# Kernel tuning notes

Hardware: AMD Instinct MI355X
Metric: run time of the kernel (lower is better)

## Reference

```python
import jax, jax.numpy as jnp
import numpy as np

B, L, D = 4, 512, 128

def setup_inputs() -> dict:
    key = jax.random.key(0)
    k1, k2, k3, k4 = jax.random.split(key, 4)
    s = 1.0 / np.sqrt(D)
    return {
        "inp": jax.random.normal(k1, (B, L, D), dtype=jnp.float32),
        "Wu": jax.random.normal(k2, (D, D), dtype=jnp.float32) * s,
        "Ww": jax.random.normal(k3, (D, D), dtype=jnp.float32) * s,
        "Wv": jax.random.normal(k4, (1, D), dtype=jnp.float32) * s,
    }

def reference(inp, Wu, Ww, Wv):
    # inp: (B,L,D); torch Linear weights are (out,in), so y = x @ W.T
    qu = inp @ Wu.T                      # (B,L,D), u(inp)
    kw = inp @ Ww.T                      # (B,L,D), w(inp)
    # qu.unsqueeze(1) -> broadcast over i; kw.unsqueeze(2) -> broadcast over j
    # h[b,i,j,:] = tanh(u(inp)[b,j] + w(inp)[b,i])   (dropout = identity in eval)
    h = jnp.tanh(qu[:, None, :, :] + kw[:, :, None, :])   # (B,L,L,D)
    score = jnp.einsum('bijd,d->bij', h, Wv[0])           # (B,L,L)
    attn = jax.nn.softmax(score, axis=2)                  # softmax over keys j
    out = jnp.einsum('bij,bjd->bid', attn, inp)           # bmm(attn, inp)
    return out, attn
```

## Files before the change

### kernel.cpp

```cpp
#include <hip/hip_runtime.h>

#define BD 128
#define SL 512
#define NB 4

__device__ __forceinline__ float rcp_fast(float x) { return __builtin_amdgcn_rcpf(x); }

__global__ __launch_bounds__(256) void k_tr(const float* __restrict__ Wu,
                                            const float* __restrict__ Ww,
                                            float* __restrict__ WuT,
                                            float* __restrict__ WwT) {
    int idx = blockIdx.x * 256 + threadIdx.x;
    int k = idx >> 7, o = idx & 127;
    WuT[idx] = Wu[o * BD + k];
    WwT[idx] = Ww[o * BD + k];
}

__global__ __launch_bounds__(256) void k_qk(const float* __restrict__ inp,
                                            const float* __restrict__ WuT,
                                            const float* __restrict__ WwT,
                                            float* __restrict__ Equ,
                                            float* __restrict__ Ekw) {
    __shared__ float sx[4][BD];
    const int t = threadIdx.x, m = t >> 7, o = t & 127;
    const int r0 = blockIdx.x * 4;
    const int b  = r0 >> 9;
    const int l0 = r0 & (SL - 1);

    #pragma unroll
    for (int h = 0; h < 2; ++h) {
        int id = h * 256 + t;
        sx[id >> 7][id & 127] = inp[(size_t)r0 * BD + id];
    }
    __syncthreads();

    const float* WT = m ? WwT : WuT;
    float acc[4] = {0.f, 0.f, 0.f, 0.f};
    #pragma unroll 8
    for (int k = 0; k < BD; ++k) {
        float w = WT[k * BD + o];
        #pragma unroll
        for (int rr = 0; rr < 4; ++rr)
            acc[rr] = fmaf(sx[rr][k], w, acc[rr]);
    }

    if (m == 0) {
        #pragma unroll
        for (int rr = 0; rr < 4; ++rr)
            Equ[(((size_t)b * 32 + (o >> 2)) * SL + (l0 + rr)) * 4 + (o & 3)] =
                __expf(2.f * acc[rr]);
    } else {
        #pragma unroll
        for (int rr = 0; rr < 4; ++rr)
            Ekw[(size_t)(r0 + rr) * BD + o] = __expf(2.f * acc[rr]);
    }
}

__global__ __launch_bounds__(1024, 4) void k_attn(const float* __restrict__ inp,
                                                  const float* __restrict__ Wv,
                                                  const float* __restrict__ Equ,
                                                  const float* __restrict__ Ekw,
                                                  float* __restrict__ out,
                                                  float* __restrict__ attn) {
    __shared__ float4 smem4[(SL * 8 + 15 * 8 * BD) / 4];
    float* smem  = (float*)smem4;
    float* s_pT  = smem;
    float* ovl   = smem + SL * 8;
    float4* s_e0 = (float4*)ovl;
    float4* s_e1 = ((float4*)ovl) + BD;
    float* s_wv  = ovl + 1024;
    float* s_ap  = ovl + 1152;
    float* s_red = ovl + 5248;
    float* s_fin = ovl;

    const int t  = threadIdx.x;
    const int b  = blockIdx.x >> 6;
    const int i0 = (blockIdx.x & 63) * 8;

    if (t < BD) {
        const float* ek = Ekw + ((size_t)b * SL + i0) * BD + t;
        s_e0[t] = make_float4(ek[0], ek[BD], ek[2 * BD], ek[3 * BD]);
        s_e1[t] = make_float4(ek[4 * BD], ek[5 * BD], ek[6 * BD], ek[7 * BD]);
        s_wv[t] = Wv[t];
    }
    __syncthreads();

    const int j = t & 511, dh = t >> 9;
    const float4* equ4 = (const float4*)(Equ + (size_t)b * BD * SL);
    float a[8] = {0.f, 0.f, 0.f, 0.f, 0.f, 0.f, 0.f, 0.f};
    #pragma unroll 4
    for (int cc = 0; cc < 16; ++cc) {
        int c = dh * 16 + cc;
        float4 q = equ4[c * SL + j];
        float qs[4] = {q.x, q.y, q.z, q.w};
        #pragma unroll
        for (int dd = 0; dd < 4; ++dd) {
            int d = c * 4 + dd;
            float4 e0 = s_e0[d];
            float4 e1 = s_e1[d];
            float  w  = s_wv[d];
            float  qd = qs[dd];
            a[0] = fmaf(w, rcp_fast(fmaf(qd, e0.x, 1.f)), a[0]);
            a[1] = fmaf(w, rcp_fast(fmaf(qd, e0.y, 1.f)), a[1]);
            a[2] = fmaf(w, rcp_fast(fmaf(qd, e0.z, 1.f)), a[2]);
            a[3] = fmaf(w, rcp_fast(fmaf(qd, e0.w, 1.f)), a[3]);
            a[4] = fmaf(w, rcp_fast(fmaf(qd, e1.x, 1.f)), a[4]);
            a[5] = fmaf(w, rcp_fast(fmaf(qd, e1.y, 1.f)), a[5]);
            a[6] = fmaf(w, rcp_fast(fmaf(qd, e1.z, 1.f)), a[6]);
            a[7] = fmaf(w, rcp_fast(fmaf(qd, e1.w, 1.f)), a[7]);
        }
    }

    const int ro = dh * 4;
    const int wo = 4 - ro;
    #pragma unroll
    for (int ii = 0; ii < 4; ++ii) s_ap[(wo + ii) * SL + j] = a[wo + ii];
    __syncthreads();
    float af[4];
    #pragma unroll
    for (int ii = 0; ii < 4; ++ii) af[ii] = a[ro + ii] + s_ap[(ro + ii) * SL + j];

    const int w8 = j >> 6;
    float mn[4];
    #pragma unroll
    for (int ii = 0; ii < 4; ++ii) mn[ii] = af[ii];
    #pragma unroll
    for (int off = 32; off > 0; off >>= 1) {
        #pragma unroll
        for (int ii = 0; ii < 4; ++ii) mn[ii] = fminf(mn[ii], __shfl_xor(mn[ii], off, 64));
    }
    if ((j & 63) == 0) {
        #pragma unroll
        for (int ii = 0; ii < 4; ++ii) s_red[(dh * 4 + ii) * 8 + w8] = mn[ii];
    }
    __syncthreads();
    #pragma unroll
    for (int ii = 0; ii < 4; ++ii) {
        float4 r0 = *(const float4*)&s_red[(dh * 4 + ii) * 8];
        float4 r1 = *(const float4*)&s_red[(dh * 4 + ii) * 8 + 4];
        mn[ii] = fminf(fminf(fminf(r0.x, r0.y), fminf(r0.z, r0.w)),
                       fminf(fminf(r1.x, r1.y), fminf(r1.z, r1.w)));
    }

    float p[4], sm[4];
    #pragma unroll
    for (int ii = 0; ii < 4; ++ii) { p[ii] = __expf(-2.f * (af[ii] - mn[ii])); sm[ii] = p[ii]; }
    #pragma unroll
    for (int off = 32; off > 0; off >>= 1) {
        #pragma unroll
        for (int ii = 0; ii < 4; ++ii) sm[ii] += __shfl_xor(sm[ii], off, 64);
    }
    __syncthreads();
    if ((j & 63) == 0) {
        #pragma unroll
        for (int ii = 0; ii < 4; ++ii) s_red[(dh * 4 + ii) * 8 + w8] = sm[ii];
    }
    __syncthreads();
    float n[4];
    #pragma unroll
    for (int ii = 0; ii < 4; ++ii) {
        float4 r0 = *(const float4*)&s_red[(dh * 4 + ii) * 8];
        float4 r1 = *(const float4*)&s_red[(dh * 4 + ii) * 8 + 4];
        float rs = rcp_fast((r0.x + r0.y) + (r0.z + r0.w) + (r1.x + r1.y) + (r1.z + r1.w));
        n[ii] = p[ii] * rs;
        attn[((size_t)b * SL + i0 + ro + ii) * SL + j] = n[ii];
    }
    ((float4*)s_pT)[j * 2 + dh] = make_float4(n[0], n[1], n[2], n[3]);
    __syncthreads();

    const int g   = t >> 6;
    const int ln  = t & 63;
    const int dq  = ln & 31;
    const int ig4 = ln >> 5;
    const float4* inp4 = (const float4*)(inp + (size_t)b * SL * BD);
    float4 acc[4];
    #pragma unroll
    for (int ii = 0; ii < 4; ++ii) acc[ii] = make_float4(0.f, 0.f, 0.f, 0.f);
    #pragma unroll 4
    for (int jj = 0; jj < 32; ++jj) {
        int jr = g * 32 + jj;
        float4 x  = inp4[jr * 32 + dq];
        float4 pp = *(const float4*)&s_pT[jr * 8 + ig4 * 4];
        acc[0].x = fmaf(pp.x, x.x, acc[0].x); acc[0].y = fmaf(pp.x, x.y, acc[0].y);
        acc[0].z = fmaf(pp.x, x.z, acc[0].z); acc[0].w = fmaf(pp.x, x.w, acc[0].w);
        acc[1].x = fmaf(pp.y, x.x, acc[1].x); acc[1].y = fmaf(pp.y, x.y, acc[1].y);
        acc[1].z = fmaf(pp.y, x.z, acc[1].z); acc[1].w = fmaf(pp.y, x.w, acc[1].w);
        acc[2].x = fmaf(pp.z, x.x, acc[2].x); acc[2].y = fmaf(pp.z, x.y, acc[2].y);
        acc[2].z = fmaf(pp.z, x.z, acc[2].z); acc[2].w = fmaf(pp.z, x.w, acc[2].w);
        acc[3].x = fmaf(pp.w, x.x, acc[3].x); acc[3].y = fmaf(pp.w, x.y, acc[3].y);
        acc[3].z = fmaf(pp.w, x.z, acc[3].z); acc[3].w = fmaf(pp.w, x.w, acc[3].w);
    }
    __syncthreads();
    if (g) {
        #pragma unroll
        for (int ii = 0; ii < 4; ++ii)
            *(float4*)&s_fin[((g - 1) * 8 + ig4 * 4 + ii) * BD + dq * 4] = acc[ii];
    }
    __syncthreads();
    if (g == 0) {
        #pragma unroll
        for (int r = 0; r < 15; ++r) {
            #pragma unroll
            for (int ii = 0; ii < 4; ++ii) {
                float4 v = *(const float4*)&s_fin[(r * 8 + ig4 * 4 + ii) * BD + dq * 4];
                acc[ii].x += v.x; acc[ii].y += v.y; acc[ii].z += v.z; acc[ii].w += v.w;
            }
        }
        #pragma unroll
        for (int ii = 0; ii < 4; ++ii)
            *(float4*)&out[((size_t)b * SL + i0 + ig4 * 4 + ii) * BD + dq * 4] = acc[ii];
    }
}

extern "C" void kernel_launch(void* const* d_in, const int* in_sizes, int n_in,
                              void* d_out, int out_size, void* d_ws, size_t ws_size,
                              hipStream_t stream) {
    const float* inp = (const float*)d_in[0];
    const float* Wu  = (const float*)d_in[1];
    const float* Ww  = (const float*)d_in[2];
    const float* Wv  = (const float*)d_in[3];

    float* out  = (float*)d_out;
    float* attn = out + (size_t)NB * SL * BD;

    float* ws  = (float*)d_ws;
    float* Equ = ws;
    float* Ekw = Equ + (size_t)NB * BD * SL;
    float* WuT = Ekw + (size_t)NB * SL * BD;
    float* WwT = WuT + BD * BD;

    k_tr  <<<BD * BD / 256, 256, 0, stream>>>(Wu, Ww, WuT, WwT);
    k_qk  <<<NB * SL / 4, 256, 0, stream>>>(inp, WuT, WwT, Equ, Ekw);
    k_attn<<<NB * SL / 8, 1024, 0, stream>>>(inp, Wv, Equ, Ekw, out, attn);
}
```

Measured before the change: 95.06 us.

## Halve query rows per attention block to double grid size and occupancy

The attention kernel now handles 4 query rows per block instead of 8, doubling the block count to 512 and raising the launch-bounds occupancy hint. Shared memory shrinks and the final cross-group reduction is redone with 512 threads summing 16 partials in parallel, replacing the serial reduction in one group. The Q/K projection kernel also reads the shared input tile as float4. The aim is better load balance and latency hiding over the CUs, at the cost of reloading Equ and inp twice as often per batch.

```diff
diff --git a/kernel.cpp b/kernel.cpp
--- a/kernel.cpp
+++ b/kernel.cpp
@@ -36,12 +36,20 @@
 
     const float* WT = m ? WwT : WuT;
     float acc[4] = {0.f, 0.f, 0.f, 0.f};
-    #pragma unroll 8
-    for (int k = 0; k < BD; ++k) {
-        float w = WT[k * BD + o];
-        #pragma unroll
-        for (int rr = 0; rr < 4; ++rr)
-            acc[rr] = fmaf(sx[rr][k], w, acc[rr]);
+    #pragma unroll 2
+    for (int k = 0; k < BD; k += 4) {
+        float w0 = WT[(k + 0) * BD + o];
+        float w1 = WT[(k + 1) * BD + o];
+        float w2 = WT[(k + 2) * BD + o];
+        float w3 = WT[(k + 3) * BD + o];
+        #pragma unroll
+        for (int rr = 0; rr < 4; ++rr) {
+            float4 x = *(const float4*)&sx[rr][k];
+            acc[rr] = fmaf(x.x, w0, acc[rr]);
+            acc[rr] = fmaf(x.y, w1, acc[rr]);
+            acc[rr] = fmaf(x.z, w2, acc[rr]);
+            acc[rr] = fmaf(x.w, w3, acc[rr]);
+        }
     }
 
     if (m == 0) {
@@ -56,38 +64,36 @@
     }
 }
 
-__global__ __launch_bounds__(1024, 4) void k_attn(const float* __restrict__ inp,
+__global__ __launch_bounds__(1024, 8) void k_attn(const float* __restrict__ inp,
                                                   const float* __restrict__ Wv,
                                                   const float* __restrict__ Equ,
                                                   const float* __restrict__ Ekw,
                                                   float* __restrict__ out,
                                                   float* __restrict__ attn) {
-    __shared__ float4 smem4[(SL * 8 + 15 * 8 * BD) / 4];
+    __shared__ float4 smem4[(SL * 4 + 16 * 4 * BD) / 4];
     float* smem  = (float*)smem4;
     float* s_pT  = smem;
-    float* ovl   = smem + SL * 8;
-    float4* s_e0 = (float4*)ovl;
-    float4* s_e1 = ((float4*)ovl) + BD;
-    float* s_wv  = ovl + 1024;
-    float* s_ap  = ovl + 1152;
-    float* s_red = ovl + 5248;
-    float* s_fin = ovl;
+    float* ovl   = smem + SL * 4;
+    float4* s_e  = (float4*)ovl;
+    float*  s_wv = ovl + 512;
+    float*  s_ap = ovl + 640;
+    float*  s_red= ovl + 640 + 4 * SL;
+    float*  s_fin= ovl;
 
     const int t  = threadIdx.x;
-    const int b  = blockIdx.x >> 6;
-    const int i0 = (blockIdx.x & 63) * 8;
+    const int b  = blockIdx.x >> 7;
+    const int i0 = (blockIdx.x & 127) * 4;
 
     if (t < BD) {
         const float* ek = Ekw + ((size_t)b * SL + i0) * BD + t;
-        s_e0[t] = make_float4(ek[0], ek[BD], ek[2 * BD], ek[3 * BD]);
-        s_e1[t] = make_float4(ek[4 * BD], ek[5 * BD], ek[6 * BD], ek[7 * BD]);
+        s_e[t]  = make_float4(ek[0], ek[BD], ek[2 * BD], ek[3 * BD]);
         s_wv[t] = Wv[t];
     }
     __syncthreads();
 
     const int j = t & 511, dh = t >> 9;
     const float4* equ4 = (const float4*)(Equ + (size_t)b * BD * SL);
-    float a[8] = {0.f, 0.f, 0.f, 0.f, 0.f, 0.f, 0.f, 0.f};
+    float a[4] = {0.f, 0.f, 0.f, 0.f};
     #pragma unroll 4
     for (int cc = 0; cc < 16; ++cc) {
         int c = dh * 16 + cc;
@@ -96,119 +102,89 @@
         #pragma unroll
         for (int dd = 0; dd < 4; ++dd) {
             int d = c * 4 + dd;
-            float4 e0 = s_e0[d];
-            float4 e1 = s_e1[d];
-            float  w  = s_wv[d];
+            float4 e = s_e[d];
+            float  w = s_wv[d];
             float  qd = qs[dd];
-            a[0] = fmaf(w, rcp_fast(fmaf(qd, e0.x, 1.f)), a[0]);
-            a[1] = fmaf(w, rcp_fast(fmaf(qd, e0.y, 1.f)), a[1]);
-            a[2] = fmaf(w, rcp_fast(fmaf(qd, e0.z, 1.f)), a[2]);
-            a[3] = fmaf(w, rcp_fast(fmaf(qd, e0.w, 1.f)), a[3]);
-            a[4] = fmaf(w, rcp_fast(fmaf(qd, e1.x, 1.f)), a[4]);
-            a[5] = fmaf(w, rcp_fast(fmaf(qd, e1.y, 1.f)), a[5]);
-            a[6] = fmaf(w, rcp_fast(fmaf(qd, e1.z, 1.f)), a[6]);
-            a[7] = fmaf(w, rcp_fast(fmaf(qd, e1.w, 1.f)), a[7]);
+            a[0] = fmaf(w, rcp_fast(fmaf(qd, e.x, 1.f)), a[0]);
+            a[1] = fmaf(w, rcp_fast(fmaf(qd, e.y, 1.f)), a[1]);
+            a[2] = fmaf(w, rcp_fast(fmaf(qd, e.z, 1.f)), a[2]);
+            a[3] = fmaf(w, rcp_fast(fmaf(qd, e.w, 1.f)), a[3]);
         }
     }
 
-    const int ro = dh * 4;
-    const int wo = 4 - ro;
-    #pragma unroll
-    for (int ii = 0; ii < 4; ++ii) s_ap[(wo + ii) * SL + j] = a[wo + ii];
-    __syncthreads();
-    float af[4];
-    #pragma unroll
-    for (int ii = 0; ii < 4; ++ii) af[ii] = a[ro + ii] + s_ap[(ro + ii) * SL + j];
+    const int ro = dh * 2, wo = 2 - ro;
+    s_ap[(wo + 0) * SL + j] = a[wo + 0];
+    s_ap[(wo + 1) * SL + j] = a[wo + 1];
+    __syncthreads();
+    float af[2] = { a[ro + 0] + s_ap[(ro + 0) * SL + j],
+                    a[ro + 1] + s_ap[(ro + 1) * SL + j] };
 
     const int w8 = j >> 6;
-    float mn[4];
-    #pragma unroll
-    for (int ii = 0; ii < 4; ++ii) mn[ii] = af[ii];
+    float mn[2] = { af[0], af[1] };
     #pragma unroll
     for (int off = 32; off > 0; off >>= 1) {
-        #pragma unroll
-        for (int ii = 0; ii < 4; ++ii) mn[ii] = fminf(mn[ii], __shfl_xor(mn[ii], off, 64));
-    }
-    if ((j & 63) == 0) {
-        #pragma unroll
-        for (int ii = 0; ii < 4; ++ii) s_red[(dh * 4 + ii) * 8 + w8] = mn[ii];
-    }
-    __syncthreads();
-    #pragma unroll
-    for (int ii = 0; ii < 4; ++ii) {
-        float4 r0 = *(const float4*)&s_red[(dh * 4 + ii) * 8];
-        float4 r1 = *(const float4*)&s_red[(dh * 4 + ii) * 8 + 4];
+        mn[0] = fminf(mn[0], __shfl_xor(mn[0], off, 64));
+        mn[1] = fminf(mn[1], __shfl_xor(mn[1], off, 64));
+    }
+    if ((j & 63) == 0) { s_red[(ro + 0) * 8 + w8] = mn[0]; s_red[(ro + 1) * 8 + w8] = mn[1]; }
+    __syncthreads();
+    #pragma unroll
+    for (int ii = 0; ii < 2; ++ii) {
+        float4 r0 = *(const float4*)&s_red[(ro + ii) * 8];
+        float4 r1 = *(const float4*)&s_red[(ro + ii) * 8 + 4];
         mn[ii] = fminf(fminf(fminf(r0.x, r0.y), fminf(r0.z, r0.w)),
                        fminf(fminf(r1.x, r1.y), fminf(r1.z, r1.w)));
     }
 
-    float p[4], sm[4];
-    #pragma unroll
-    for (int ii = 0; ii < 4; ++ii) { p[ii] = __expf(-2.f * (af[ii] - mn[ii])); sm[ii] = p[ii]; }
+    float p[2] = { __expf(-2.f * (af[0] - mn[0])), __expf(-2.f * (af[1] - mn[1])) };
+    float sm[2] = { p[0], p[1] };
     #pragma unroll
     for (int off = 32; off > 0; off >>= 1) {
-        #pragma unroll
-        for (int ii = 0; ii < 4; ++ii) sm[ii] += __shfl_xor(sm[ii], off, 64);
-    }
-    __syncthreads();
-    if ((j & 63) == 0) {
-        #pragma unroll
-        for (int ii = 0; ii < 4; ++ii) s_red[(dh * 4 + ii) * 8 + w8] = sm[ii];
-    }
-    __syncthreads();
-    float n[4];
-    #pragma unroll
-    for (int ii = 0; ii < 4; ++ii) {
-        float4 r0 = *(const float4*)&s_red[(dh * 4 + ii) * 8];
-        float4 r1 = *(const float4*)&s_red[(dh * 4 + ii) * 8 + 4];
+        sm[0] += __shfl_xor(sm[0], off, 64);
+        sm[1] += __shfl_xor(sm[1], off, 64);
+    }
+    __syncthreads();
+    if ((j & 63) == 0) { s_red[(ro + 0) * 8 + w8] = sm[0]; s_red[(ro + 1) * 8 + w8] = sm[1]; }
+    __syncthreads();
+    float n[2];
+    #pragma unroll
+    for (int ii = 0; ii < 2; ++ii) {
+        float4 r0 = *(const float4*)&s_red[(ro + ii) * 8];
+        float4 r1 = *(const float4*)&s_red[(ro + ii) * 8 + 4];
         float rs = rcp_fast((r0.x + r0.y) + (r0.z + r0.w) + (r1.x + r1.y) + (r1.z + r1.w));
         n[ii] = p[ii] * rs;
         attn[((size_t)b * SL + i0 + ro + ii) * SL + j] = n[ii];
     }
-    ((float4*)s_pT)[j * 2 + dh] = make_float4(n[0], n[1], n[2], n[3]);
-    __syncthreads();
-
-    const int g   = t >> 6;
-    const int ln  = t & 63;
-    const int dq  = ln & 31;
-    const int ig4 = ln >> 5;
+    ((float2*)s_pT)[j * 2 + dh] = make_float2(n[0], n[1]);
+    __syncthreads();
+
+    const int g  = t >> 6;
+    const int ln = t & 63;
+    const int dq = ln & 31;
+    const int rh = ln >> 5;
     const float4* inp4 = (const float4*)(inp + (size_t)b * SL * BD);
-    float4 acc[4];
-    #pragma unroll
-    for (int ii = 0; ii < 4; ++ii) acc[ii] = make_float4(0.f, 0.f, 0.f, 0.f);
+    float4 acc0 = make_float4(0.f, 0.f, 0.f, 0.f);
+    float4 acc1 = make_float4(0.f, 0.f, 0.f, 0.f);
     #pragma unroll 4
     for (int jj = 0; jj < 32; ++jj) {
         int jr = g * 32 + jj;
         float4 x  = inp4[jr * 32 + dq];
-        float4 pp = *(const float4*)&s_pT[jr * 8 + ig4 * 4];
-        acc[0].x = fmaf(pp.x, x.x, acc[0].x); acc[0].y = fmaf(pp.x, x.y, acc[0].y);
-        acc[0].z = fmaf(pp.x, x.z, acc[0].z); acc[0].w = fmaf(pp.x, x.w, acc[0].w);
-        acc[1].x = fmaf(pp.y, x.x, acc[1].x); acc[1].y = fmaf(pp.y, x.y, acc[1].y);
-        acc[1].z = fmaf(pp.y, x.z, acc[1].z); acc[1].w = fmaf(pp.y, x.w, acc[1].w);
-        acc[2].x = fmaf(pp.z, x.x, acc[2].x); acc[2].y = fmaf(pp.z, x.y, acc[2].y);
-        acc[2].z = fmaf(pp.z, x.z, acc[2].z); acc[2].w = fmaf(pp.z, x.w, acc[2].w);
-        acc[3].x = fmaf(pp.w, x.x, acc[3].x); acc[3].y = fmaf(pp.w, x.y, acc[3].y);
-        acc[3].z = fmaf(pp.w, x.z, acc[3].z); acc[3].w = fmaf(pp.w, x.w, acc[3].w);
-    }
-    __syncthreads();
-    if (g) {
-        #pragma unroll
-        for (int ii = 0; ii < 4; ++ii)
-            *(float4*)&s_fin[((g - 1) * 8 + ig4 * 4 + ii) * BD + dq * 4] = acc[ii];
-    }
-    __syncthreads();
-    if (g == 0) {
-        #pragma unroll
-        for (int r = 0; r < 15; ++r) {
-            #pragma unroll
-            for (int ii = 0; ii < 4; ++ii) {
-                float4 v = *(const float4*)&s_fin[(r * 8 + ig4 * 4 + ii) * BD + dq * 4];
-                acc[ii].x += v.x; acc[ii].y += v.y; acc[ii].z += v.z; acc[ii].w += v.w;
-            }
-        }
-        #pragma unroll
-        for (int ii = 0; ii < 4; ++ii)
-            *(float4*)&out[((size_t)b * SL + i0 + ig4 * 4 + ii) * BD + dq * 4] = acc[ii];
+        float2 pp = ((const float2*)s_pT)[jr * 2 + rh];
+        acc0.x = fmaf(pp.x, x.x, acc0.x); acc0.y = fmaf(pp.x, x.y, acc0.y);
+        acc0.z = fmaf(pp.x, x.z, acc0.z); acc0.w = fmaf(pp.x, x.w, acc0.w);
+        acc1.x = fmaf(pp.y, x.x, acc1.x); acc1.y = fmaf(pp.y, x.y, acc1.y);
+        acc1.z = fmaf(pp.y, x.z, acc1.z); acc1.w = fmaf(pp.y, x.w, acc1.w);
+    }
+    *(float4*)&s_fin[((g * 4) + rh * 2 + 0) * BD + dq * 4] = acc0;
+    *(float4*)&s_fin[((g * 4) + rh * 2 + 1) * BD + dq * 4] = acc1;
+    __syncthreads();
+    if (t < 512) {
+        int row = t >> 7, d = t & 127;
+        float s = 0.f;
+        #pragma unroll
+        for (int gg = 0; gg < 16; ++gg)
+            s += s_fin[(gg * 4 + row) * BD + d];
+        out[((size_t)b * SL + i0 + row) * BD + d] = s;
     }
 }
 
@@ -231,5 +207,5 @@
 
     k_tr  <<<BD * BD / 256, 256, 0, stream>>>(Wu, Ww, WuT, WwT);
     k_qk  <<<NB * SL / 4, 256, 0, stream>>>(inp, WuT, WwT, Equ, Ekw);
-    k_attn<<<NB * SL / 8, 1024, 0, stream>>>(inp, Wv, Equ, Ekw, out, attn);
-}
+    k_attn<<<NB * SL / 4, 1024, 0, stream>>>(inp, Wv, Equ, Ekw, out, attn);
+}
```

After: 95.83 us. No clear change (+0.8%).
